# Performance work log

Hardware: AMD Instinct MI355X
Metric: run time of the kernel (lower is better)

## Reference

```python
import jax, jax.numpy as jnp
import numpy as np

GRID = 10          # 10x10 Battleship board -> 100 nodes
HIDDEN = 128
B = 2048
LN_EPS = 1e-5


def _build_grid_edges():
    """Directed 4-neighbor edges on a GRIDxGRID board, with a scalar dir feature."""
    src, dst, ed = [], [], []
    dirs = [(-1, 0), (1, 0), (0, -1), (0, 1)]  # up, down, left, right
    for r in range(GRID):
        for c in range(GRID):
            u = r * GRID + c
            for d, (dr, dc) in enumerate(dirs):
                rr, cc = r + dr, c + dc
                if 0 <= rr < GRID and 0 <= cc < GRID:
                    src.append(u)
                    dst.append(rr * GRID + cc)
                    ed.append(d / 3.0)
    return (np.asarray(src, np.int32), np.asarray(dst, np.int32),
            np.asarray(ed, np.float32)[:, None])


def setup_inputs() -> dict:
    key = jax.random.key(0)
    ks = jax.random.split(key, 8)
    src, dst, ed = _build_grid_edges()  # 360 edges
    H = HIDDEN
    s1 = 1.0 / np.sqrt(H + 1)
    s2 = 1.0 / np.sqrt(H)
    s3 = 1.0 / np.sqrt(2 * H)
    return {
        "x": jax.random.normal(ks[0], (B, GRID * GRID, H), jnp.float32),
        "src_idx": jnp.asarray(src),
        "dst_idx": jnp.asarray(dst),
        "edge_dir": jnp.asarray(ed),
        "w_msg1": jax.random.normal(ks[1], (H + 1, H), jnp.float32) * s1,
        "b_msg1": jnp.zeros((H,), jnp.float32),
        "w_msg2": jax.random.normal(ks[2], (H, H), jnp.float32) * s2,
        "b_msg2": jnp.zeros((H,), jnp.float32),
        "w_upd1": jax.random.normal(ks[3], (2 * H, H), jnp.float32) * s3,
        "b_upd1": jnp.zeros((H,), jnp.float32),
        "w_upd2": jax.random.normal(ks[4], (H, H), jnp.float32) * s2,
        "b_upd2": jnp.zeros((H,), jnp.float32),
        "gamma": jnp.ones((H,), jnp.float32),
        "beta": jnp.zeros((H,), jnp.float32),
    }


def reference(x, src_idx, dst_idx, edge_dir,
              w_msg1, b_msg1, w_msg2, b_msg2,
              w_upd1, b_upd1, w_upd2, b_upd2,
              gamma, beta):
    Bsz, n_nodes, H = x.shape
    E = src_idx.shape[0]
    # gather source node states: [B, E, H]
    x_src = x[:, src_idx, :]
    # edge features broadcast over batch: [B, E, 1]
    ef = jnp.broadcast_to(edge_dir[None], (Bsz, E, edge_dir.shape[-1]))
    # message MLP: Linear -> ReLU -> Linear
    m = jnp.concatenate([x_src, ef], axis=-1)
    m = jax.nn.relu(jnp.einsum('beh,hk->bek', m, w_msg1) + b_msg1)
    messages = jnp.einsum('beh,hk->bek', m, w_msg2) + b_msg2
    # scatter-add aggregate into per-node buffer: [B, N, H]
    agg = jnp.zeros((Bsz, n_nodes, H), x.dtype).at[:, dst_idx, :].add(messages)
    # update MLP on concat([x, agg])
    u = jnp.concatenate([x, agg], axis=-1)
    u = jax.nn.relu(jnp.einsum('bnh,hk->bnk', u, w_upd1) + b_upd1)
    u = jnp.einsum('bnh,hk->bnk', u, w_upd2) + b_upd2
    # residual + LayerNorm
    h = x + u
    mu = jnp.mean(h, axis=-1, keepdims=True)
    var = jnp.mean(jnp.square(h - mu), axis=-1, keepdims=True)
    return (h - mu) * jax.lax.rsqrt(var + LN_EPS) * gamma + beta
```

## Files before the change

### kernel.cpp

```cpp
#include <hip/hip_runtime.h>

#define NNODE 100
#define HDIM  128
#define NEDGE 360
#define NT    512

typedef float f32x4 __attribute__((ext_vector_type(4)));
typedef short s16x8 __attribute__((ext_vector_type(8)));

__device__ __forceinline__ float bf2f(short s) {
  union { unsigned int u; float f; } v;
  v.u = ((unsigned int)(unsigned short)s) << 16;
  return v.f;
}
__device__ __forceinline__ short f2bf(float f) {
  union { float f; unsigned int u; } v; v.f = f;
  unsigned int u = v.u + 0x7fffu + ((v.u >> 16) & 1u);
  return (short)(u >> 16);
}
__device__ __forceinline__ int sidx(int r, int k) {
  return (r << 7) + ((((k >> 3) ^ (r & 15)) << 3) | (k & 7));
}

__global__ __launch_bounds__(NT)
void prep_tr(const float* __restrict__ w_msg1, const float* __restrict__ w_upd1,
             const float* __restrict__ w_upd2, const int* __restrict__ dst_idx,
             short* __restrict__ wt, int* __restrict__ inl) {
  int idx = blockIdx.x * NT + threadIdx.x;
  if (idx < 3 * 16384) {
    int m = idx >> 14, i = idx & 16383;
    int n = i >> 7, k = i & 127;
    const float* W = (m == 0) ? w_msg1 : (m == 1) ? w_upd1 : w_upd2;
    int slot = (m == 0) ? 0 : (m == 1) ? 2 : 3;
    wt[slot * 16384 + n * HDIM + k] = f2bf(W[k * HDIM + n]);
  }
  if (blockIdx.x == 0) {
    __shared__ int cnt[NNODE];
    int tid = threadIdx.x;
    if (tid < NNODE) cnt[tid] = 0;
    __syncthreads();
    if (tid < NEDGE) {
      int d = dst_idx[tid];
      int p = atomicAdd(&cnt[d], 1);
      inl[d * 4 + p] = tid;
    }
    __syncthreads();
    if (tid < NNODE) {
      for (int p = cnt[tid]; p < 4; ++p) inl[tid * 4 + p] = -1;
    }
  }
}

__global__ __launch_bounds__(128)
void prep_fold(const float* __restrict__ w_msg2, const float* __restrict__ w_upd1,
               const float* __restrict__ b_msg2,
               short* __restrict__ wt, float* __restrict__ bv) {
  const int j = threadIdx.x;
  if (blockIdx.x < 128) {
    const int i = blockIdx.x;
    float s = 0.f;
#pragma unroll 4
    for (int k = 0; k < 128; ++k)
      s += w_msg2[i * HDIM + k] * w_upd1[(HDIM + k) * HDIM + j];
    wt[16384 + j * HDIM + i] = f2bf(s);
  } else {
    float s = 0.f;
#pragma unroll 4
    for (int k = 0; k < 128; ++k)
      s += b_msg2[k] * w_upd1[(HDIM + k) * HDIM + j];
    bv[j] = s;
  }
}

__global__ __launch_bounds__(NT, 4)
void mpnn_main(const float* __restrict__ x,
               const int* __restrict__ src_idx,
               const float* __restrict__ edge_dir,
               const float* __restrict__ w_msg1,
               const float* __restrict__ b_msg1,
               const float* __restrict__ b_upd1,
               const float* __restrict__ b_upd2,
               const float* __restrict__ gamma,
               const float* __restrict__ beta,
               const short* __restrict__ wt,
               const float* __restrict__ bv_g,
               const int* __restrict__ inl_g,
               float* __restrict__ out)
{
  __shared__ __align__(16) char smem[69184];
  short* buf0 = (short*)smem;
  short* buf1 = (short*)(smem + 25600);
  float* lnb  = (float*)(smem + 58368);
  int*   srcl = (int*)(smem + 60416);
  float* eds  = (float*)(smem + 61952);
  int*   inls = (int*)(smem + 63488);
  float* cntf = (float*)(smem + 65088);
  float* b1s  = (float*)(smem + 65600);
  float* w1ls = (float*)(smem + 66112);
  float* bvs  = (float*)(smem + 66624);
  float* bu1s = (float*)(smem + 67136);
  float* bu2s = (float*)(smem + 67648);
  float* gms  = (float*)(smem + 68160);
  float* bts  = (float*)(smem + 68672);

  const int tid  = threadIdx.x;
  const int lane = tid & 63;
  const int wave = tid >> 6;
  const int quad = lane >> 4;
  const int l16  = lane & 15;
  const int wr   = wave >> 1;
  const int wc   = wave & 1;
  const int b    = blockIdx.x;
  const float* xb = x + (size_t)b * (NNODE * HDIM);

  s16x8 wf[4][4];
  auto loadB = [&](const short* w) {
#pragma unroll
    for (int ct = 0; ct < 4; ++ct)
#pragma unroll
      for (int kq = 0; kq < 4; ++kq)
        wf[ct][kq] = *(const s16x8*)&w[(wc * 64 + ct * 16 + l16) * HDIM + kq * 32 + quad * 8];
  };

  loadB(wt);
  for (int G = tid; G < NNODE * 16; G += NT) {
    int r = G >> 4, g = G & 15;
    const float4* p = (const float4*)(xb + r * HDIM + g * 8);
    float4 v0 = p[0], v1 = p[1];
    s16x8 h;
    h[0] = f2bf(v0.x); h[1] = f2bf(v0.y); h[2] = f2bf(v0.z); h[3] = f2bf(v0.w);
    h[4] = f2bf(v1.x); h[5] = f2bf(v1.y); h[6] = f2bf(v1.z); h[7] = f2bf(v1.w);
    *(s16x8*)&buf0[sidx(r, g * 8)] = h;
  }
  if (tid < 384) {
    srcl[tid] = (tid < NEDGE) ? src_idx[tid] : 0;
    eds[tid]  = (tid < NEDGE) ? edge_dir[tid] : 0.f;
  }
  if (tid < NNODE) {
    int4 il = ((const int4*)inl_g)[tid];
    ((int4*)inls)[tid] = il;
    cntf[tid] = (float)((il.x >= 0) + (il.y >= 0) + (il.z >= 0) + (il.w >= 0));
  } else if (tid < HDIM) {
    cntf[tid] = 0.f;
  }
  if (tid < HDIM) {
    b1s[tid]  = b_msg1[tid];
    w1ls[tid] = w_msg1[HDIM * HDIM + tid];
    bvs[tid]  = bv_g[tid];
    bu1s[tid] = b_upd1[tid];
    bu2s[tid] = b_upd2[tid];
    gms[tid]  = gamma[tid];
    bts[tid]  = beta[tid];
  }
  __syncthreads();

  const int r0 = wr * 32 + l16;
  const int r1 = r0 + 16;
  const int m0 = (r0 < NNODE) ? r0 : 0;
  const int m1 = (r1 < NNODE) ? r1 : 0;

  {
    f32x4 acc[2][4] = {};
#pragma unroll
    for (int kq = 0; kq < 4; ++kq) {
      const int ko = kq * 32 + quad * 8;
      s16x8 a0 = *(const s16x8*)&buf0[sidx(m0, ko)];
      s16x8 a1 = *(const s16x8*)&buf0[sidx(m1, ko)];
#pragma unroll
      for (int ct = 0; ct < 4; ++ct) {
        acc[0][ct] = __builtin_amdgcn_mfma_f32_16x16x32_bf16(a0, wf[ct][kq], acc[0][ct], 0, 0, 0);
        acc[1][ct] = __builtin_amdgcn_mfma_f32_16x16x32_bf16(a1, wf[ct][kq], acc[1][ct], 0, 0, 0);
      }
    }
    loadB(wt + 16384);
#pragma unroll
    for (int rt = 0; rt < 2; ++rt)
#pragma unroll
      for (int i = 0; i < 4; ++i) {
        const int row = wr * 32 + rt * 16 + quad * 4 + i;
#pragma unroll
        for (int ct = 0; ct < 4; ++ct) {
          const int col = wc * 64 + ct * 16 + l16;
          buf1[sidx(row, col)] = f2bf(acc[rt][ct][i]);
        }
      }
  }
  __syncthreads();

  for (int G = tid; G < NNODE * 16; G += NT) {
    const int v = G >> 4, ko = (G & 15) * 8;
    const int4 il = ((const int4*)inls)[v];
    const float4 ba = *(const float4*)&b1s[ko];
    const float4 bb = *(const float4*)&b1s[ko + 4];
    const float4 wa = *(const float4*)&w1ls[ko];
    const float4 wb = *(const float4*)&w1ls[ko + 4];
    float s[8] = {0, 0, 0, 0, 0, 0, 0, 0};
    const int es[4] = {il.x, il.y, il.z, il.w};
#pragma unroll
    for (int j = 0; j < 4; ++j) {
      if (es[j] >= 0) {
        const int e = es[j];
        const float ed = eds[e];
        s16x8 t8 = *(const s16x8*)&buf1[sidx(srcl[e], ko)];
        float u;
        u = bf2f(t8[0]) + ba.x + ed * wa.x; s[0] += u > 0.f ? u : 0.f;
        u = bf2f(t8[1]) + ba.y + ed * wa.y; s[1] += u > 0.f ? u : 0.f;
        u = bf2f(t8[2]) + ba.z + ed * wa.z; s[2] += u > 0.f ? u : 0.f;
        u = bf2f(t8[3]) + ba.w + ed * wa.w; s[3] += u > 0.f ? u : 0.f;
        u = bf2f(t8[4]) + bb.x + ed * wb.x; s[4] += u > 0.f ? u : 0.f;
        u = bf2f(t8[5]) + bb.y + ed * wb.y; s[5] += u > 0.f ? u : 0.f;
        u = bf2f(t8[6]) + bb.z + ed * wb.z; s[6] += u > 0.f ? u : 0.f;
        u = bf2f(t8[7]) + bb.w + ed * wb.w; s[7] += u > 0.f ? u : 0.f;
      }
    }
    s16x8 o;
#pragma unroll
    for (int t = 0; t < 8; ++t) o[t] = f2bf(s[t]);
    *(s16x8*)&buf0[sidx(v, ko)] = o;
  }
  __syncthreads();

  {
    f32x4 acc[2][4] = {};
#pragma unroll
    for (int kq = 0; kq < 4; ++kq) {
      const int ko = kq * 32 + quad * 8;
      s16x8 a0 = *(const s16x8*)&buf0[sidx(m0, ko)];
      s16x8 a1 = *(const s16x8*)&buf0[sidx(m1, ko)];
#pragma unroll
      for (int ct = 0; ct < 4; ++ct) {
        acc[0][ct] = __builtin_amdgcn_mfma_f32_16x16x32_bf16(a0, wf[ct][kq], acc[0][ct], 0, 0, 0);
        acc[1][ct] = __builtin_amdgcn_mfma_f32_16x16x32_bf16(a1, wf[ct][kq], acc[1][ct], 0, 0, 0);
      }
    }
    loadB(wt + 2 * 16384);
#pragma unroll
    for (int kq = 0; kq < 4; ++kq) {
      const int ko = kq * 32 + quad * 8;
#pragma unroll
      for (int rt = 0; rt < 2; ++rt) {
        const int rr = rt ? m1 : m0;
        const float4* p = (const float4*)(xb + rr * HDIM + ko);
        float4 v0 = p[0], v1 = p[1];
        s16x8 a;
        a[0] = f2bf(v0.x); a[1] = f2bf(v0.y); a[2] = f2bf(v0.z); a[3] = f2bf(v0.w);
        a[4] = f2bf(v1.x); a[5] = f2bf(v1.y); a[6] = f2bf(v1.z); a[7] = f2bf(v1.w);
#pragma unroll
        for (int ct = 0; ct < 4; ++ct)
          acc[rt][ct] = __builtin_amdgcn_mfma_f32_16x16x32_bf16(a, wf[ct][kq], acc[rt][ct], 0, 0, 0);
      }
    }
    loadB(wt + 3 * 16384);
#pragma unroll
    for (int rt = 0; rt < 2; ++rt)
#pragma unroll
      for (int i = 0; i < 4; ++i) {
        const int row = wr * 32 + rt * 16 + quad * 4 + i;
        const float cn = cntf[row];
#pragma unroll
        for (int ct = 0; ct < 4; ++ct) {
          const int col = wc * 64 + ct * 16 + l16;
          float v = acc[rt][ct][i] + bu1s[col] + cn * bvs[col];
          buf1[sidx(row, col)] = f2bf(v > 0.f ? v : 0.f);
        }
      }
  }
  __syncthreads();

  {
    f32x4 acc[2][4] = {};
#pragma unroll
    for (int kq = 0; kq < 4; ++kq) {
      const int ko = kq * 32 + quad * 8;
      s16x8 a0 = *(const s16x8*)&buf1[sidx(wr * 32 + l16, ko)];
      s16x8 a1 = *(const s16x8*)&buf1[sidx(wr * 32 + 16 + l16, ko)];
#pragma unroll
      for (int ct = 0; ct < 4; ++ct) {
        acc[0][ct] = __builtin_amdgcn_mfma_f32_16x16x32_bf16(a0, wf[ct][kq], acc[0][ct], 0, 0, 0);
        acc[1][ct] = __builtin_amdgcn_mfma_f32_16x16x32_bf16(a1, wf[ct][kq], acc[1][ct], 0, 0, 0);
      }
    }
#pragma unroll
    for (int rt = 0; rt < 2; ++rt)
#pragma unroll
      for (int i = 0; i < 4; ++i) {
        const int row = wr * 32 + rt * 16 + quad * 4 + i;
        if (row < NNODE) {
          float s1 = 0.f, s2 = 0.f;
#pragma unroll
          for (int ct = 0; ct < 4; ++ct) {
            const int col = wc * 64 + ct * 16 + l16;
            const float h = acc[rt][ct][i] + bu2s[col] + xb[row * HDIM + col];
            acc[rt][ct][i] = h;
            s1 += h; s2 += h * h;
          }
#pragma unroll
          for (int off = 8; off > 0; off >>= 1) {
            s1 += __shfl_xor(s1, off, 64);
            s2 += __shfl_xor(s2, off, 64);
          }
          if (l16 == 0) { lnb[(row * 2 + wc) * 2] = s1; lnb[(row * 2 + wc) * 2 + 1] = s2; }
        }
      }
    __syncthreads();
#pragma unroll
    for (int rt = 0; rt < 2; ++rt)
#pragma unroll
      for (int i = 0; i < 4; ++i) {
        const int row = wr * 32 + rt * 16 + quad * 4 + i;
        if (row < NNODE) {
          const float s1 = lnb[row * 4] + lnb[row * 4 + 2];
          const float s2 = lnb[row * 4 + 1] + lnb[row * 4 + 3];
          const float mu  = s1 * (1.0f / HDIM);
          const float var = s2 * (1.0f / HDIM) - mu * mu;
          const float rs  = rsqrtf(var + 1e-5f);
#pragma unroll
          for (int ct = 0; ct < 4; ++ct) {
            const int col = wc * 64 + ct * 16 + l16;
            out[((size_t)b * NNODE + row) * HDIM + col] =
                (acc[rt][ct][i] - mu) * rs * gms[col] + bts[col];
          }
        }
      }
  }
}

extern "C" void kernel_launch(void* const* d_in, const int* in_sizes, int n_in,
                              void* d_out, int out_size, void* d_ws, size_t ws_size,
                              hipStream_t stream) {
  const float* x      = (const float*)d_in[0];
  const int*   src    = (const int*)  d_in[1];
  const int*   dst    = (const int*)  d_in[2];
  const float* ed     = (const float*)d_in[3];
  const float* w_msg1 = (const float*)d_in[4];
  const float* b_msg1 = (const float*)d_in[5];
  const float* w_msg2 = (const float*)d_in[6];
  const float* b_msg2 = (const float*)d_in[7];
  const float* w_upd1 = (const float*)d_in[8];
  const float* b_upd1 = (const float*)d_in[9];
  const float* w_upd2 = (const float*)d_in[10];
  const float* b_upd2 = (const float*)d_in[11];
  const float* gamma  = (const float*)d_in[12];
  const float* beta   = (const float*)d_in[13];
  float* out = (float*)d_out;

  short* wt  = (short*)d_ws;
  float* bv  = (float*)((char*)d_ws + 131072);
  int*   inl = (int*)((char*)d_ws + 131584);

  prep_tr<<<96, NT, 0, stream>>>(w_msg1, w_upd1, w_upd2, dst, wt, inl);
  prep_fold<<<129, 128, 0, stream>>>(w_msg2, w_upd1, b_msg2, wt, bv);

  const int Bsz = in_sizes[0] / (NNODE * HDIM);
  mpnn_main<<<Bsz, NT, 0, stream>>>(x, src, ed, w_msg1, b_msg1,
                                    b_upd1, b_upd2, gamma, beta, wt, bv, inl, out);
}
```

Measured before the change: 434.6 us.

## Keep x fragments in registers, stage LayerNorm output through LDS for vector stores

Converts x to bf16 MFMA A-fragments once into registers and reuses them for both the message GEMM and the update GEMM, removing the LDS staging pass, one barrier and the second global read of x. The residual x values are prefetched into registers before the final GEMM rather than loaded in the epilogue. The LayerNorm output is written to a swizzled fp32 LDS tile so each thread can emit coalesced float4 global stores instead of scattered scalar stores. This raises register pressure under the 4-blocks-per-SM launch bound and shrinks LDS use.

```diff
diff --git a/kernel.cpp b/kernel.cpp
--- a/kernel.cpp
+++ b/kernel.cpp
@@ -20,6 +20,9 @@
 }
 __device__ __forceinline__ int sidx(int r, int k) {
   return (r << 7) + ((((k >> 3) ^ (r & 15)) << 3) | (k & 7));
+}
+__device__ __forceinline__ int hidx(int r, int c) {
+  return (r << 7) + (c ^ ((r & 4) << 2));
 }
 
 __global__ __launch_bounds__(NT)
@@ -87,21 +90,22 @@
                const int* __restrict__ inl_g,
                float* __restrict__ out)
 {
-  __shared__ __align__(16) char smem[69184];
-  short* buf0 = (short*)smem;
-  short* buf1 = (short*)(smem + 25600);
-  float* lnb  = (float*)(smem + 58368);
-  int*   srcl = (int*)(smem + 60416);
-  float* eds  = (float*)(smem + 61952);
-  int*   inls = (int*)(smem + 63488);
-  float* cntf = (float*)(smem + 65088);
-  float* b1s  = (float*)(smem + 65600);
-  float* w1ls = (float*)(smem + 66112);
-  float* bvs  = (float*)(smem + 66624);
-  float* bu1s = (float*)(smem + 67136);
-  float* bu2s = (float*)(smem + 67648);
-  float* gms  = (float*)(smem + 68160);
-  float* bts  = (float*)(smem + 68672);
+  __shared__ __align__(16) char smem[61568];
+  short* bufT = (short*)smem;
+  short* bufM = (short*)(smem + 25600);
+  float* hbuf = (float*)smem;
+  float* lnb  = (float*)(smem + 51200);
+  int*   srcl = (int*)(smem + 52800);
+  float* eds  = (float*)(smem + 54336);
+  int*   inls = (int*)(smem + 55872);
+  float* cntf = (float*)(smem + 57472);
+  float* b1s  = (float*)(smem + 57984);
+  float* w1ls = (float*)(smem + 58496);
+  float* bvs  = (float*)(smem + 59008);
+  float* bu1s = (float*)(smem + 59520);
+  float* bu2s = (float*)(smem + 60032);
+  float* gms  = (float*)(smem + 60544);
+  float* bts  = (float*)(smem + 61056);
 
   const int tid  = threadIdx.x;
   const int lane = tid & 63;
@@ -113,6 +117,11 @@
   const int b    = blockIdx.x;
   const float* xb = x + (size_t)b * (NNODE * HDIM);
 
+  const int r0 = wr * 32 + l16;
+  const int r1 = r0 + 16;
+  const int m0 = (r0 < NNODE) ? r0 : 0;
+  const int m1 = (r1 < NNODE) ? r1 : 0;
+
   s16x8 wf[4][4];
   auto loadB = [&](const short* w) {
 #pragma unroll
@@ -123,14 +132,20 @@
   };
 
   loadB(wt);
-  for (int G = tid; G < NNODE * 16; G += NT) {
-    int r = G >> 4, g = G & 15;
-    const float4* p = (const float4*)(xb + r * HDIM + g * 8);
-    float4 v0 = p[0], v1 = p[1];
-    s16x8 h;
-    h[0] = f2bf(v0.x); h[1] = f2bf(v0.y); h[2] = f2bf(v0.z); h[3] = f2bf(v0.w);
-    h[4] = f2bf(v1.x); h[5] = f2bf(v1.y); h[6] = f2bf(v1.z); h[7] = f2bf(v1.w);
-    *(s16x8*)&buf0[sidx(r, g * 8)] = h;
+  s16x8 xa[2][4];
+#pragma unroll
+  for (int kq = 0; kq < 4; ++kq) {
+    const int ko = kq * 32 + quad * 8;
+#pragma unroll
+    for (int rt = 0; rt < 2; ++rt) {
+      const int rr = rt ? m1 : m0;
+      const float4* p = (const float4*)(xb + rr * HDIM + ko);
+      float4 v0 = p[0], v1 = p[1];
+      s16x8 a;
+      a[0] = f2bf(v0.x); a[1] = f2bf(v0.y); a[2] = f2bf(v0.z); a[3] = f2bf(v0.w);
+      a[4] = f2bf(v1.x); a[5] = f2bf(v1.y); a[6] = f2bf(v1.z); a[7] = f2bf(v1.w);
+      xa[rt][kq] = a;
+    }
   }
   if (tid < 384) {
     srcl[tid] = (tid < NEDGE) ? src_idx[tid] : 0;
@@ -152,36 +167,30 @@
     gms[tid]  = gamma[tid];
     bts[tid]  = beta[tid];
   }
-  __syncthreads();
-
-  const int r0 = wr * 32 + l16;
-  const int r1 = r0 + 16;
-  const int m0 = (r0 < NNODE) ? r0 : 0;
-  const int m1 = (r1 < NNODE) ? r1 : 0;
+
+  f32x4 xr[2][4];
 
   {
     f32x4 acc[2][4] = {};
 #pragma unroll
-    for (int kq = 0; kq < 4; ++kq) {
-      const int ko = kq * 32 + quad * 8;
-      s16x8 a0 = *(const s16x8*)&buf0[sidx(m0, ko)];
-      s16x8 a1 = *(const s16x8*)&buf0[sidx(m1, ko)];
+    for (int kq = 0; kq < 4; ++kq)
 #pragma unroll
       for (int ct = 0; ct < 4; ++ct) {
-        acc[0][ct] = __builtin_amdgcn_mfma_f32_16x16x32_bf16(a0, wf[ct][kq], acc[0][ct], 0, 0, 0);
-        acc[1][ct] = __builtin_amdgcn_mfma_f32_16x16x32_bf16(a1, wf[ct][kq], acc[1][ct], 0, 0, 0);
-      }
-    }
+        acc[0][ct] = __builtin_amdgcn_mfma_f32_16x16x32_bf16(xa[0][kq], wf[ct][kq], acc[0][ct], 0, 0, 0);
+        acc[1][ct] = __builtin_amdgcn_mfma_f32_16x16x32_bf16(xa[1][kq], wf[ct][kq], acc[1][ct], 0, 0, 0);
+      }
     loadB(wt + 16384);
 #pragma unroll
     for (int rt = 0; rt < 2; ++rt)
 #pragma unroll
       for (int i = 0; i < 4; ++i) {
         const int row = wr * 32 + rt * 16 + quad * 4 + i;
-#pragma unroll
-        for (int ct = 0; ct < 4; ++ct) {
-          const int col = wc * 64 + ct * 16 + l16;
-          buf1[sidx(row, col)] = f2bf(acc[rt][ct][i]);
+        if (row < NNODE) {
+#pragma unroll
+          for (int ct = 0; ct < 4; ++ct) {
+            const int col = wc * 64 + ct * 16 + l16;
+            bufT[sidx(row, col)] = f2bf(acc[rt][ct][i]);
+          }
         }
       }
   }
@@ -201,7 +210,7 @@
       if (es[j] >= 0) {
         const int e = es[j];
         const float ed = eds[e];
-        s16x8 t8 = *(const s16x8*)&buf1[sidx(srcl[e], ko)];
+        s16x8 t8 = *(const s16x8*)&bufT[sidx(srcl[e], ko)];
         float u;
         u = bf2f(t8[0]) + ba.x + ed * wa.x; s[0] += u > 0.f ? u : 0.f;
         u = bf2f(t8[1]) + ba.y + ed * wa.y; s[1] += u > 0.f ? u : 0.f;
@@ -216,7 +225,7 @@
     s16x8 o;
 #pragma unroll
     for (int t = 0; t < 8; ++t) o[t] = f2bf(s[t]);
-    *(s16x8*)&buf0[sidx(v, ko)] = o;
+    *(s16x8*)&bufM[sidx(v, ko)] = o;
   }
   __syncthreads();
 
@@ -225,8 +234,8 @@
 #pragma unroll
     for (int kq = 0; kq < 4; ++kq) {
       const int ko = kq * 32 + quad * 8;
-      s16x8 a0 = *(const s16x8*)&buf0[sidx(m0, ko)];
-      s16x8 a1 = *(const s16x8*)&buf0[sidx(m1, ko)];
+      s16x8 a0 = *(const s16x8*)&bufM[sidx(m0, ko)];
+      s16x8 a1 = *(const s16x8*)&bufM[sidx(m1, ko)];
 #pragma unroll
       for (int ct = 0; ct < 4; ++ct) {
         acc[0][ct] = __builtin_amdgcn_mfma_f32_16x16x32_bf16(a0, wf[ct][kq], acc[0][ct], 0, 0, 0);
@@ -235,51 +244,57 @@
     }
     loadB(wt + 2 * 16384);
 #pragma unroll
+    for (int kq = 0; kq < 4; ++kq)
+#pragma unroll
+      for (int ct = 0; ct < 4; ++ct) {
+        acc[0][ct] = __builtin_amdgcn_mfma_f32_16x16x32_bf16(xa[0][kq], wf[ct][kq], acc[0][ct], 0, 0, 0);
+        acc[1][ct] = __builtin_amdgcn_mfma_f32_16x16x32_bf16(xa[1][kq], wf[ct][kq], acc[1][ct], 0, 0, 0);
+      }
+    loadB(wt + 3 * 16384);
+#pragma unroll
+    for (int rt = 0; rt < 2; ++rt)
+#pragma unroll
+      for (int i = 0; i < 4; ++i) {
+        const int row = wr * 32 + rt * 16 + quad * 4 + i;
+        const int rr = (row < NNODE) ? row : 0;
+#pragma unroll
+        for (int ct = 0; ct < 4; ++ct) {
+          const int col = wc * 64 + ct * 16 + l16;
+          xr[rt][ct][i] = xb[rr * HDIM + col];
+        }
+      }
+#pragma unroll
+    for (int rt = 0; rt < 2; ++rt)
+#pragma unroll
+      for (int i = 0; i < 4; ++i) {
+        const int row = wr * 32 + rt * 16 + quad * 4 + i;
+        if (row < NNODE) {
+          const float cn = cntf[row];
+#pragma unroll
+          for (int ct = 0; ct < 4; ++ct) {
+            const int col = wc * 64 + ct * 16 + l16;
+            float v = acc[rt][ct][i] + bu1s[col] + cn * bvs[col];
+            bufT[sidx(row, col)] = f2bf(v > 0.f ? v : 0.f);
+          }
+        }
+      }
+  }
+  __syncthreads();
+
+  {
+    f32x4 acc[2][4] = {};
+#pragma unroll
     for (int kq = 0; kq < 4; ++kq) {
       const int ko = kq * 32 + quad * 8;
-#pragma unroll
-      for (int rt = 0; rt < 2; ++rt) {
-        const int rr = rt ? m1 : m0;
-        const float4* p = (const float4*)(xb + rr * HDIM + ko);
-        float4 v0 = p[0], v1 = p[1];
-        s16x8 a;
-        a[0] = f2bf(v0.x); a[1] = f2bf(v0.y); a[2] = f2bf(v0.z); a[3] = f2bf(v0.w);
-        a[4] = f2bf(v1.x); a[5] = f2bf(v1.y); a[6] = f2bf(v1.z); a[7] = f2bf(v1.w);
-#pragma unroll
-        for (int ct = 0; ct < 4; ++ct)
-          acc[rt][ct] = __builtin_amdgcn_mfma_f32_16x16x32_bf16(a, wf[ct][kq], acc[rt][ct], 0, 0, 0);
-      }
-    }
-    loadB(wt + 3 * 16384);
-#pragma unroll
-    for (int rt = 0; rt < 2; ++rt)
-#pragma unroll
-      for (int i = 0; i < 4; ++i) {
-        const int row = wr * 32 + rt * 16 + quad * 4 + i;
-        const float cn = cntf[row];
-#pragma unroll
-        for (int ct = 0; ct < 4; ++ct) {
-          const int col = wc * 64 + ct * 16 + l16;
-          float v = acc[rt][ct][i] + bu1s[col] + cn * bvs[col];
-          buf1[sidx(row, col)] = f2bf(v > 0.f ? v : 0.f);
-        }
-      }
-  }
-  __syncthreads();
-
-  {
-    f32x4 acc[2][4] = {};
-#pragma unroll
-    for (int kq = 0; kq < 4; ++kq) {
-      const int ko = kq * 32 + quad * 8;
-      s16x8 a0 = *(const s16x8*)&buf1[sidx(wr * 32 + l16, ko)];
-      s16x8 a1 = *(const s16x8*)&buf1[sidx(wr * 32 + 16 + l16, ko)];
+      s16x8 a0 = *(const s16x8*)&bufT[sidx(m0, ko)];
+      s16x8 a1 = *(const s16x8*)&bufT[sidx(m1, ko)];
 #pragma unroll
       for (int ct = 0; ct < 4; ++ct) {
         acc[0][ct] = __builtin_amdgcn_mfma_f32_16x16x32_bf16(a0, wf[ct][kq], acc[0][ct], 0, 0, 0);
         acc[1][ct] = __builtin_amdgcn_mfma_f32_16x16x32_bf16(a1, wf[ct][kq], acc[1][ct], 0, 0, 0);
       }
     }
+    __syncthreads();
 #pragma unroll
     for (int rt = 0; rt < 2; ++rt)
 #pragma unroll
@@ -290,8 +305,8 @@
 #pragma unroll
           for (int ct = 0; ct < 4; ++ct) {
             const int col = wc * 64 + ct * 16 + l16;
-            const float h = acc[rt][ct][i] + bu2s[col] + xb[row * HDIM + col];
-            acc[rt][ct][i] = h;
+            const float h = acc[rt][ct][i] + bu2s[col] + xr[rt][ct][i];
+            hbuf[hidx(row, col)] = h;
             s1 += h; s2 += h * h;
           }
 #pragma unroll
@@ -299,29 +314,28 @@
             s1 += __shfl_xor(s1, off, 64);
             s2 += __shfl_xor(s2, off, 64);
           }
-          if (l16 == 0) { lnb[(row * 2 + wc) * 2] = s1; lnb[(row * 2 + wc) * 2 + 1] = s2; }
+          if (l16 == 0) { lnb[row * 4 + wc * 2] = s1; lnb[row * 4 + wc * 2 + 1] = s2; }
         }
       }
     __syncthreads();
-#pragma unroll
-    for (int rt = 0; rt < 2; ++rt)
-#pragma unroll
-      for (int i = 0; i < 4; ++i) {
-        const int row = wr * 32 + rt * 16 + quad * 4 + i;
-        if (row < NNODE) {
-          const float s1 = lnb[row * 4] + lnb[row * 4 + 2];
-          const float s2 = lnb[row * 4 + 1] + lnb[row * 4 + 3];
-          const float mu  = s1 * (1.0f / HDIM);
-          const float var = s2 * (1.0f / HDIM) - mu * mu;
-          const float rs  = rsqrtf(var + 1e-5f);
-#pragma unroll
-          for (int ct = 0; ct < 4; ++ct) {
-            const int col = wc * 64 + ct * 16 + l16;
-            out[((size_t)b * NNODE + row) * HDIM + col] =
-                (acc[rt][ct][i] - mu) * rs * gms[col] + bts[col];
-          }
-        }
-      }
+    for (int G = tid; G < NNODE * 32; G += NT) {
+      const int row = G >> 5;
+      const int c = (G & 31) * 4;
+      const float4 h = *(const float4*)&hbuf[hidx(row, c)];
+      const float s1 = lnb[row * 4] + lnb[row * 4 + 2];
+      const float s2 = lnb[row * 4 + 1] + lnb[row * 4 + 3];
+      const float mu  = s1 * (1.0f / HDIM);
+      const float var = s2 * (1.0f / HDIM) - mu * mu;
+      const float rs  = rsqrtf(var + 1e-5f);
+      const float4 g  = *(const float4*)&gms[c];
+      const float4 bt = *(const float4*)&bts[c];
+      float4 o;
+      o.x = (h.x - mu) * rs * g.x + bt.x;
+      o.y = (h.y - mu) * rs * g.y + bt.y;
+      o.z = (h.z - mu) * rs * g.z + bt.z;
+      o.w = (h.w - mu) * rs * g.w + bt.w;
+      *(float4*)&out[((size_t)b * NNODE + row) * HDIM + c] = o;
+    }
   }
 }
 
```

Result: slower. 475.6 us (+9.4%).
